# Kernel optimization log

Hardware: AMD Instinct MI355X
Metric: run time of the kernel (lower is better)

Reference implementation:

```python
import jax, jax.numpy as jnp
import numpy as np

N_NODES = 10242  # icosphere level-5 node count
NNZ = 71694      # ~7 nonzeros per row (6 neighbors + self)


def setup_inputs() -> dict:
    key = jax.random.key(0)
    k1, k2, k3, k4, k5 = jax.random.split(key, 5)
    B, T, C, Cout, Ks = 2, 16, 16, 32, 20
    x = jax.random.normal(k1, (B, T, N_NODES, C), dtype=jnp.float32)
    edge_row = jax.random.randint(k2, (NNZ,), 0, N_NODES, dtype=jnp.int32)
    edge_col = jax.random.randint(k3, (NNZ,), 0, N_NODES, dtype=jnp.int32)
    # small values keep the Chebyshev recurrence numerically bounded over Ks steps
    edge_val = jax.random.uniform(k4, (NNZ,), dtype=jnp.float32, minval=-0.2, maxval=0.2)
    W = jax.random.normal(k5, (Cout, C * Ks), dtype=jnp.float32) * 0.02
    return {"x": x, "edge_row": edge_row, "edge_col": edge_col,
            "edge_val": edge_val, "W": W}


def reference(x, edge_row, edge_col, edge_val, W):
    B, T, N, C = x.shape
    Cout, CK = W.shape
    Ks = CK // C

    def spmm(v):  # sparse L @ v, v: [N, F]
        return jax.ops.segment_sum(edge_val[:, None] * v[edge_col], edge_row,
                                   num_segments=N)

    # [B,T,N,C] -> [B*T,N,C] -> [N,C,B*T] -> [N, C*B*T]
    x0 = x.reshape(B * T, N, C).transpose(1, 2, 0).reshape(N, C * B * T)
    x1 = spmm(x0)

    def step(carry, _):
        a, b = carry
        c = 2.0 * spmm(b) - a
        return (b, c), c

    _, rest = jax.lax.scan(step, (x0, x1), None, length=Ks - 2)
    xs = jnp.concatenate([x0[None], x1[None], rest], axis=0)  # [Ks, N, C*B*T]

    xs = xs.reshape(Ks, N, C, B * T).transpose(3, 1, 2, 0)  # [B*T, N, C, Ks]
    xs = xs.reshape(B * T * N, C * Ks)
    out = xs @ W.T  # [B*T*N, Cout]
    return out.reshape(B, T, N, Cout)
```

## Files before the change

### kernel.cpp

```cpp
#include <hip/hip_runtime.h>

#define N_NODES 10242
#define NNZ_E   71694
#define NNZ_PAD_MAX (NNZ_E + 3 * N_NODES)
#define BT      32
#define C_IN    16
#define K_S     20
#define C_OUT   32
#define F       512
typedef unsigned short u16;
typedef unsigned int   u32;

#define RING_ELEMS ((size_t)N_NODES * F)
#define RING_BYTES (RING_ELEMS * 2)
#define R_SLOTS    8

typedef __attribute__((ext_vector_type(8)))  _Float16 half8;
typedef __attribute__((ext_vector_type(16))) float    float16;

__device__ __forceinline__ void unpack8h(uint4 u, float* f) {
    union { uint4 u; _Float16 h[8]; } v; v.u = u;
    #pragma unroll
    for (int i = 0; i < 8; ++i) f[i] = (float)v.h[i];
}
__device__ __forceinline__ uint4 pack8h(const float* f) {
    union { uint4 u; _Float16 h[8]; } v;
    #pragma unroll
    for (int i = 0; i < 8; ++i) v.h[i] = (_Float16)f[i];
    return v.u;
}
__device__ __forceinline__ u16 f2h(float f) {
    union { _Float16 h; u16 u; } v; v.h = (_Float16)f; return v.u;
}


__global__ void zero_kernel(int* p, int n) {
    int i = blockIdx.x * blockDim.x + threadIdx.x;
    if (i < n) p[i] = 0;
}

__global__ void count_kernel(const int* __restrict__ erow, int* cnt) {
    int e = blockIdx.x * blockDim.x + threadIdx.x;
    if (e < NNZ_E) atomicAdd(&cnt[erow[e]], 1);
}

__global__ void scan_kernel(const int* __restrict__ cnt, int* row_ptr, int* cursor) {
    const int T = 256;
    const int chunk = (N_NODES + T - 1) / T;
    __shared__ int part[T];
    int t = threadIdx.x;
    int base = t * chunk;
    int s = 0;
    for (int i = 0; i < chunk; ++i) {
        int idx = base + i;
        if (idx < N_NODES) s += (cnt[idx] + 3) & ~3;
    }
    part[t] = s;
    __syncthreads();
    for (int off = 1; off < T; off <<= 1) {
        int v = (t >= off) ? part[t - off] : 0;
        __syncthreads();
        part[t] += v;
        __syncthreads();
    }
    int run = (t == 0) ? 0 : part[t - 1];
    for (int i = 0; i < chunk; ++i) {
        int idx = base + i;
        if (idx < N_NODES) {
            row_ptr[idx] = run;
            cursor[idx]  = run;
            run += (cnt[idx] + 3) & ~3;
        }
    }
    if (base <= N_NODES && N_NODES < base + chunk) {
        row_ptr[N_NODES] = run;
    }
}

__global__ void scatter_kernel(const int* __restrict__ erow, int* cursor, int* __restrict__ eidx) {
    int e = blockIdx.x * blockDim.x + threadIdx.x;
    if (e < NNZ_E) {
        int p = atomicAdd(&cursor[erow[e]], 1);
        eidx[p] = e;
    }
}

__global__ void sort_rows_kernel(const int* __restrict__ row_ptr, const int* __restrict__ cnt,
                                 int* eidx) {
    int r = blockIdx.x * blockDim.x + threadIdx.x;
    if (r >= N_NODES) return;
    int s = row_ptr[r], e = s + cnt[r];
    for (int i = s + 1; i < e; ++i) {
        int key = eidx[i];
        int j = i - 1;
        while (j >= s && eidx[j] > key) { eidx[j + 1] = eidx[j]; --j; }
        eidx[j + 1] = key;
    }
}

__global__ void fill_csr_kernel(const int* __restrict__ row_ptr, const int* __restrict__ cnt,
                                const int* __restrict__ eidx,
                                const int* __restrict__ ecol, const float* __restrict__ eval,
                                int2* __restrict__ cpack) {
    int r = blockIdx.x * blockDim.x + threadIdx.x;
    if (r >= N_NODES) return;
    int s = row_ptr[r], e = s + cnt[r];
    for (int p = s; p < e; ++p) {
        int ed = eidx[p];
        cpack[p] = make_int2(ecol[ed], __float_as_int(eval[ed]));
    }
}

__global__ void wtfrag_kernel(const float* __restrict__ W, u16* __restrict__ wtfrag) {
    int i = blockIdx.x * blockDim.x + threadIdx.x;
    if (i >= K_S * 64 * 8) return;
    int j    = i & 7;
    int lane = (i >> 3) & 63;
    int k    = i >> 9;
    int cout = lane & 31;
    int c    = ((lane >> 5) << 3) + j;
    wtfrag[i] = f2h(W[cout * (C_IN * K_S) + c * K_S + k]);
}


__global__ __launch_bounds__(256) void transform_kernel(
        const float* __restrict__ x, u16* __restrict__ T0) {
    int g = blockIdx.x * 256 + threadIdx.x;
    int n   = g >> 9;
    int rem = g & 511;
    int bt  = rem >> 4;
    int c   = rem & 15;
    float v = x[((size_t)bt * N_NODES + n) * C_IN + c];
    T0[(size_t)n * F + rem] = f2h(v);
}


__global__ __launch_bounds__(64) void spmm_step_kernel(
        const u16* __restrict__ srcB, const u16* __restrict__ srcA,
        u16* __restrict__ dst,
        const int* __restrict__ row_ptr, const int2* __restrict__ cpack,
        float alpha, float beta) {
    int n = blockIdx.x;
    int lane = threadIdx.x;
    int s = row_ptr[n], e_end = row_ptr[n + 1];

    float a[8] = {0,0,0,0,0,0,0,0};
    if (beta != 0.f) {
        uint4 ua = ((const uint4*)(srcA + (size_t)n * F))[lane];
        unpack8h(ua, a);
    }

    float acc0[8] = {0,0,0,0,0,0,0,0};
    float acc1[8] = {0,0,0,0,0,0,0,0};

    for (int e = s; e < e_end; e += 4) {
        int2 p0 = cpack[e + 0], p1 = cpack[e + 1];
        int2 p2 = cpack[e + 2], p3 = cpack[e + 3];
        uint4 g0 = ((const uint4*)(srcB + (size_t)p0.x * F))[lane];
        uint4 g1 = ((const uint4*)(srcB + (size_t)p1.x * F))[lane];
        uint4 g2 = ((const uint4*)(srcB + (size_t)p2.x * F))[lane];
        uint4 g3 = ((const uint4*)(srcB + (size_t)p3.x * F))[lane];
        float b0[8], b1[8], b2[8], b3[8];
        unpack8h(g0, b0); unpack8h(g1, b1); unpack8h(g2, b2); unpack8h(g3, b3);
        float v0 = __int_as_float(p0.y), v1 = __int_as_float(p1.y);
        float v2 = __int_as_float(p2.y), v3 = __int_as_float(p3.y);
        #pragma unroll
        for (int i = 0; i < 8; ++i) {
            acc0[i] += v0 * b0[i];
            acc1[i] += v1 * b1[i];
            acc0[i] += v2 * b2[i];
            acc1[i] += v3 * b3[i];
        }
    }

    float y[8];
    #pragma unroll
    for (int i = 0; i < 8; ++i)
        y[i] = alpha * (acc0[i] + acc1[i]) + beta * a[i];

    ((uint4*)(dst + (size_t)n * F))[lane] = pack8h(y);
}


__global__ __launch_bounds__(256) void proj_mfma_kernel(
        const u16* __restrict__ ring, int k0, int kcnt,
        const u16* __restrict__ wtfrag, float* __restrict__ out, int accumulate) {
    int wave = threadIdx.x >> 6;
    int lane = threadIdx.x & 63;
    int n = blockIdx.x * 4 + wave;
    if (n >= N_NODES) return;

    int col = lane & 31;
    int grp = lane >> 5;
    size_t aoff = (size_t)n * F + (size_t)col * 16 + grp * 8;

    union { uint4 u; half8 h; } av[8], bv[8];
    #pragma unroll
    for (int j = 0; j < 8; ++j) {
        int jj = (j < kcnt) ? j : 0;
        int k = k0 + jj;
        av[j].u = *(const uint4*)(ring + (size_t)(k % R_SLOTS) * RING_ELEMS + aoff);
        bv[j].u = *(const uint4*)(wtfrag + (size_t)k * 512 + lane * 8);
    }

    float16 acc = {};
    #pragma unroll
    for (int j = 0; j < 8; ++j) {
        if (j < kcnt)
            acc = __builtin_amdgcn_mfma_f32_32x32x16_f16(av[j].h, bv[j].h, acc, 0, 0, 0);
    }

    #pragma unroll
    for (int r = 0; r < 16; ++r) {
        int bt = (r & 3) + 8 * (r >> 2) + 4 * grp;
        float* op = out + ((size_t)bt * N_NODES + n) * C_OUT + col;
        if (accumulate) *op += acc[r];
        else            *op  = acc[r];
    }
}


extern "C" void kernel_launch(void* const* d_in, const int* in_sizes, int n_in,
                              void* d_out, int out_size, void* d_ws, size_t ws_size,
                              hipStream_t stream) {
    const float* x    = (const float*)d_in[0];
    const int*   erow = (const int*)  d_in[1];
    const int*   ecol = (const int*)  d_in[2];
    const float* eval = (const float*)d_in[3];
    const float* W    = (const float*)d_in[4];
    float* out = (float*)d_out;

    char* ws = (char*)d_ws;
    size_t o = 0;
    auto alloc = [&](size_t bytes) -> char* {
        o = (o + 511) & ~(size_t)511;
        char* r = ws + o;
        o += bytes;
        return r;
    };
    int*   cnt     = (int*)  alloc((size_t)N_NODES * 4);
    int*   row_ptr = (int*)  alloc((size_t)(N_NODES + 1) * 4);
    int*   cursor  = (int*)  alloc((size_t)N_NODES * 4);
    int*   eidx    = (int*)  alloc((size_t)NNZ_PAD_MAX * 4);
    int2*  cpack   = (int2*) alloc((size_t)NNZ_PAD_MAX * 8);
    u16*   wtfrag  = (u16*)  alloc((size_t)K_S * 512 * 2);

    u16* ring = (u16*)alloc((size_t)R_SLOTS * RING_BYTES);
    auto slot = [&](int k) -> u16* { return ring + (size_t)(k % R_SLOTS) * RING_ELEMS; };

    zero_kernel<<<(N_NODES + 255) / 256, 256, 0, stream>>>(cnt, N_NODES);
    zero_kernel<<<(2 * NNZ_PAD_MAX + 255) / 256, 256, 0, stream>>>((int*)cpack, 2 * NNZ_PAD_MAX);
    count_kernel<<<(NNZ_E + 255) / 256, 256, 0, stream>>>(erow, cnt);
    scan_kernel<<<1, 256, 0, stream>>>(cnt, row_ptr, cursor);
    scatter_kernel<<<(NNZ_E + 255) / 256, 256, 0, stream>>>(erow, cursor, eidx);
    sort_rows_kernel<<<(N_NODES + 255) / 256, 256, 0, stream>>>(row_ptr, cnt, eidx);
    fill_csr_kernel<<<(N_NODES + 255) / 256, 256, 0, stream>>>(row_ptr, cnt, eidx, ecol, eval, cpack);
    wtfrag_kernel<<<(K_S * 512 + 255) / 256, 256, 0, stream>>>(W, wtfrag);

    const int proj_blocks = (N_NODES + 3) / 4;
    int c0 = 0;
    auto maybe_pass = [&](int k_done) {
        int target = K_S - c0;
        if (target > R_SLOTS) target = R_SLOTS;
        if (target > 0 && (k_done - c0 + 1) == target) {
            proj_mfma_kernel<<<proj_blocks, 256, 0, stream>>>(
                ring, c0, target, wtfrag, out, (c0 > 0) ? 1 : 0);
            c0 += target;
        }
    };

    transform_kernel<<<(int)(RING_ELEMS / 256), 256, 0, stream>>>(x, slot(0));
    maybe_pass(0);

    for (int k = 1; k < K_S; ++k) {
        const u16* srcB = slot(k - 1);
        const u16* srcA = (k >= 2) ? slot(k - 2) : slot(k - 1);
        float alpha = (k == 1) ? 1.f : 2.f;
        float beta  = (k == 1) ? 0.f : -1.f;
        spmm_step_kernel<<<N_NODES, 64, 0, stream>>>(
            srcB, srcA, slot(k), row_ptr, cpack, alpha, beta);
        maybe_pass(k);
    }
}
```

Measured before the change: 491.4 us.

## Fuse CSR build into one block, pad rows to 2, widen ring to 10 slots

Replaces the eight-kernel CSR setup with a single 1024-thread block that counts, scans, scatters, sorts and packs in shared memory, and folds the weight-fragment packing into the transform kernel. Row padding drops from multiples of 4 to multiples of 2, and the SpMM loop is unrolled by 2 to match, cutting wasted zero-edge gathers. The ring grows to 10 slots so the projection runs in two passes instead of three, and the projection kernel now software-pipelines its loads around the MFMA loop. The single-block CSR build serialises setup work on one CU, which may cost more than the launches it removes.

```diff
diff --git a/kernel.cpp b/kernel.cpp
--- a/kernel.cpp
+++ b/kernel.cpp
@@ -2,7 +2,7 @@
 
 #define N_NODES 10242
 #define NNZ_E   71694
-#define NNZ_PAD_MAX (NNZ_E + 3 * N_NODES)
+#define NNZ_PAD_MAX (NNZ_E + N_NODES)
 #define BT      32
 #define C_IN    16
 #define K_S     20
@@ -13,7 +13,7 @@
 
 #define RING_ELEMS ((size_t)N_NODES * F)
 #define RING_BYTES (RING_ELEMS * 2)
-#define R_SLOTS    8
+#define R_SLOTS    10
 
 typedef __attribute__((ext_vector_type(8)))  _Float16 half8;
 typedef __attribute__((ext_vector_type(16))) float    float16;
@@ -34,30 +34,30 @@
 }
 
 
-__global__ void zero_kernel(int* p, int n) {
-    int i = blockIdx.x * blockDim.x + threadIdx.x;
-    if (i < n) p[i] = 0;
-}
-
-__global__ void count_kernel(const int* __restrict__ erow, int* cnt) {
-    int e = blockIdx.x * blockDim.x + threadIdx.x;
-    if (e < NNZ_E) atomicAdd(&cnt[erow[e]], 1);
-}
-
-__global__ void scan_kernel(const int* __restrict__ cnt, int* row_ptr, int* cursor) {
-    const int T = 256;
-    const int chunk = (N_NODES + T - 1) / T;
-    __shared__ int part[T];
+__global__ __launch_bounds__(1024) void csr_build_kernel(
+        const int* __restrict__ erow, const int* __restrict__ ecol,
+        const float* __restrict__ eval,
+        int* __restrict__ row_ptr, int* __restrict__ eidx,
+        int2* __restrict__ cpack) {
+    __shared__ int cur[N_NODES];
+    __shared__ int part[1024];
     int t = threadIdx.x;
+
+    for (int i = t; i < N_NODES; i += 1024) cur[i] = 0;
+    __syncthreads();
+    for (int e = t; e < NNZ_E; e += 1024) atomicAdd(&cur[erow[e]], 1);
+    __syncthreads();
+
+    const int chunk = (N_NODES + 1023) / 1024;
     int base = t * chunk;
     int s = 0;
     for (int i = 0; i < chunk; ++i) {
         int idx = base + i;
-        if (idx < N_NODES) s += (cnt[idx] + 3) & ~3;
+        if (idx < N_NODES) s += (cur[idx] + 1) & ~1;
     }
     part[t] = s;
     __syncthreads();
-    for (int off = 1; off < T; off <<= 1) {
+    for (int off = 1; off < 1024; off <<= 1) {
         int v = (t >= off) ? part[t - off] : 0;
         __syncthreads();
         part[t] += v;
@@ -67,65 +67,52 @@
     for (int i = 0; i < chunk; ++i) {
         int idx = base + i;
         if (idx < N_NODES) {
+            int c = cur[idx];
             row_ptr[idx] = run;
-            cursor[idx]  = run;
-            run += (cnt[idx] + 3) & ~3;
-        }
-    }
-    if (base <= N_NODES && N_NODES < base + chunk) {
-        row_ptr[N_NODES] = run;
-    }
-}
-
-__global__ void scatter_kernel(const int* __restrict__ erow, int* cursor, int* __restrict__ eidx) {
-    int e = blockIdx.x * blockDim.x + threadIdx.x;
-    if (e < NNZ_E) {
-        int p = atomicAdd(&cursor[erow[e]], 1);
+            cur[idx] = run;
+            run += (c + 1) & ~1;
+        }
+    }
+    if (base <= N_NODES && N_NODES < base + chunk) row_ptr[N_NODES] = run;
+    __syncthreads();
+
+    for (int e = t; e < NNZ_E; e += 1024) {
+        int p = atomicAdd(&cur[erow[e]], 1);
         eidx[p] = e;
     }
-}
-
-__global__ void sort_rows_kernel(const int* __restrict__ row_ptr, const int* __restrict__ cnt,
-                                 int* eidx) {
-    int r = blockIdx.x * blockDim.x + threadIdx.x;
-    if (r >= N_NODES) return;
-    int s = row_ptr[r], e = s + cnt[r];
-    for (int i = s + 1; i < e; ++i) {
-        int key = eidx[i];
-        int j = i - 1;
-        while (j >= s && eidx[j] > key) { eidx[j + 1] = eidx[j]; --j; }
-        eidx[j + 1] = key;
-    }
-}
-
-__global__ void fill_csr_kernel(const int* __restrict__ row_ptr, const int* __restrict__ cnt,
-                                const int* __restrict__ eidx,
-                                const int* __restrict__ ecol, const float* __restrict__ eval,
-                                int2* __restrict__ cpack) {
-    int r = blockIdx.x * blockDim.x + threadIdx.x;
-    if (r >= N_NODES) return;
-    int s = row_ptr[r], e = s + cnt[r];
-    for (int p = s; p < e; ++p) {
-        int ed = eidx[p];
-        cpack[p] = make_int2(ecol[ed], __float_as_int(eval[ed]));
-    }
-}
-
-__global__ void wtfrag_kernel(const float* __restrict__ W, u16* __restrict__ wtfrag) {
-    int i = blockIdx.x * blockDim.x + threadIdx.x;
-    if (i >= K_S * 64 * 8) return;
-    int j    = i & 7;
-    int lane = (i >> 3) & 63;
-    int k    = i >> 9;
-    int cout = lane & 31;
-    int c    = ((lane >> 5) << 3) + j;
-    wtfrag[i] = f2h(W[cout * (C_IN * K_S) + c * K_S + k]);
+    __syncthreads();
+
+    for (int r = t; r < N_NODES; r += 1024) {
+        int st = row_ptr[r];
+        int en = cur[r];
+        int pe = row_ptr[r + 1];
+        for (int i = st + 1; i < en; ++i) {
+            int key = eidx[i];
+            int j = i - 1;
+            while (j >= st && eidx[j] > key) { eidx[j + 1] = eidx[j]; --j; }
+            eidx[j + 1] = key;
+        }
+        for (int p = st; p < en; ++p) {
+            int ed = eidx[p];
+            cpack[p] = make_int2(ecol[ed], __float_as_int(eval[ed]));
+        }
+        for (int p = en; p < pe; ++p) cpack[p] = make_int2(0, 0);
+    }
 }
 
 
 __global__ __launch_bounds__(256) void transform_kernel(
-        const float* __restrict__ x, u16* __restrict__ T0) {
+        const float* __restrict__ x, const float* __restrict__ W,
+        u16* __restrict__ T0, u16* __restrict__ wtfrag) {
     int g = blockIdx.x * 256 + threadIdx.x;
+    if (g < K_S * 512) {
+        int j    = g & 7;
+        int lane = (g >> 3) & 63;
+        int k    = g >> 9;
+        int cout = lane & 31;
+        int c    = ((lane >> 5) << 3) + j;
+        wtfrag[g] = f2h(W[cout * (C_IN * K_S) + c * K_S + k]);
+    }
     int n   = g >> 9;
     int rem = g & 511;
     int bt  = rem >> 4;
@@ -144,32 +131,26 @@
     int lane = threadIdx.x;
     int s = row_ptr[n], e_end = row_ptr[n + 1];
 
-    float a[8] = {0,0,0,0,0,0,0,0};
+    float a[8] = {0, 0, 0, 0, 0, 0, 0, 0};
     if (beta != 0.f) {
         uint4 ua = ((const uint4*)(srcA + (size_t)n * F))[lane];
         unpack8h(ua, a);
     }
 
-    float acc0[8] = {0,0,0,0,0,0,0,0};
-    float acc1[8] = {0,0,0,0,0,0,0,0};
-
-    for (int e = s; e < e_end; e += 4) {
-        int2 p0 = cpack[e + 0], p1 = cpack[e + 1];
-        int2 p2 = cpack[e + 2], p3 = cpack[e + 3];
+    float acc0[8] = {0, 0, 0, 0, 0, 0, 0, 0};
+    float acc1[8] = {0, 0, 0, 0, 0, 0, 0, 0};
+
+    for (int e = s; e < e_end; e += 2) {
+        int2 p0 = cpack[e], p1 = cpack[e + 1];
         uint4 g0 = ((const uint4*)(srcB + (size_t)p0.x * F))[lane];
         uint4 g1 = ((const uint4*)(srcB + (size_t)p1.x * F))[lane];
-        uint4 g2 = ((const uint4*)(srcB + (size_t)p2.x * F))[lane];
-        uint4 g3 = ((const uint4*)(srcB + (size_t)p3.x * F))[lane];
-        float b0[8], b1[8], b2[8], b3[8];
-        unpack8h(g0, b0); unpack8h(g1, b1); unpack8h(g2, b2); unpack8h(g3, b3);
+        float b0[8], b1[8];
+        unpack8h(g0, b0); unpack8h(g1, b1);
         float v0 = __int_as_float(p0.y), v1 = __int_as_float(p1.y);
-        float v2 = __int_as_float(p2.y), v3 = __int_as_float(p3.y);
         #pragma unroll
         for (int i = 0; i < 8; ++i) {
             acc0[i] += v0 * b0[i];
             acc1[i] += v1 * b1[i];
-            acc0[i] += v2 * b2[i];
-            acc1[i] += v3 * b3[i];
         }
     }
 
@@ -194,20 +175,21 @@
     int grp = lane >> 5;
     size_t aoff = (size_t)n * F + (size_t)col * 16 + grp * 8;
 
-    union { uint4 u; half8 h; } av[8], bv[8];
-    #pragma unroll
-    for (int j = 0; j < 8; ++j) {
-        int jj = (j < kcnt) ? j : 0;
-        int k = k0 + jj;
-        av[j].u = *(const uint4*)(ring + (size_t)(k % R_SLOTS) * RING_ELEMS + aoff);
-        bv[j].u = *(const uint4*)(wtfrag + (size_t)k * 512 + lane * 8);
-    }
+    union uv { uint4 u; half8 h; };
+    uv av, bv;
+    av.u = *(const uint4*)(ring + (size_t)(k0 % R_SLOTS) * RING_ELEMS + aoff);
+    bv.u = *(const uint4*)(wtfrag + (size_t)k0 * 512 + lane * 8);
 
     float16 acc = {};
-    #pragma unroll
-    for (int j = 0; j < 8; ++j) {
-        if (j < kcnt)
-            acc = __builtin_amdgcn_mfma_f32_32x32x16_f16(av[j].h, bv[j].h, acc, 0, 0, 0);
+    for (int j = 0; j < kcnt; ++j) {
+        uv an = av, bn = bv;
+        if (j + 1 < kcnt) {
+            int k = k0 + j + 1;
+            an.u = *(const uint4*)(ring + (size_t)(k % R_SLOTS) * RING_ELEMS + aoff);
+            bn.u = *(const uint4*)(wtfrag + (size_t)k * 512 + lane * 8);
+        }
+        acc = __builtin_amdgcn_mfma_f32_32x32x16_f16(av.h, bv.h, acc, 0, 0, 0);
+        av = an; bv = bn;
     }
 
     #pragma unroll
@@ -238,24 +220,16 @@
         o += bytes;
         return r;
     };
-    int*   cnt     = (int*)  alloc((size_t)N_NODES * 4);
     int*   row_ptr = (int*)  alloc((size_t)(N_NODES + 1) * 4);
-    int*   cursor  = (int*)  alloc((size_t)N_NODES * 4);
     int*   eidx    = (int*)  alloc((size_t)NNZ_PAD_MAX * 4);
     int2*  cpack   = (int2*) alloc((size_t)NNZ_PAD_MAX * 8);
     u16*   wtfrag  = (u16*)  alloc((size_t)K_S * 512 * 2);
-
-    u16* ring = (u16*)alloc((size_t)R_SLOTS * RING_BYTES);
+    u16*   ring    = (u16*)  alloc((size_t)R_SLOTS * RING_BYTES);
     auto slot = [&](int k) -> u16* { return ring + (size_t)(k % R_SLOTS) * RING_ELEMS; };
 
-    zero_kernel<<<(N_NODES + 255) / 256, 256, 0, stream>>>(cnt, N_NODES);
-    zero_kernel<<<(2 * NNZ_PAD_MAX + 255) / 256, 256, 0, stream>>>((int*)cpack, 2 * NNZ_PAD_MAX);
-    count_kernel<<<(NNZ_E + 255) / 256, 256, 0, stream>>>(erow, cnt);
-    scan_kernel<<<1, 256, 0, stream>>>(cnt, row_ptr, cursor);
-    scatter_kernel<<<(NNZ_E + 255) / 256, 256, 0, stream>>>(erow, cursor, eidx);
-    sort_rows_kernel<<<(N_NODES + 255) / 256, 256, 0, stream>>>(row_ptr, cnt, eidx);
-    fill_csr_kernel<<<(N_NODES + 255) / 256, 256, 0, stream>>>(row_ptr, cnt, eidx, ecol, eval, cpack);
-    wtfrag_kernel<<<(K_S * 512 + 255) / 256, 256, 0, stream>>>(W, wtfrag);
+    csr_build_kernel<<<1, 1024, 0, stream>>>(erow, ecol, eval, row_ptr, eidx, cpack);
+
+    transform_kernel<<<(int)(RING_ELEMS / 256), 256, 0, stream>>>(x, W, slot(0), wtfrag);
 
     const int proj_blocks = (N_NODES + 3) / 4;
     int c0 = 0;
@@ -264,12 +238,11 @@
         if (target > R_SLOTS) target = R_SLOTS;
         if (target > 0 && (k_done - c0 + 1) == target) {
             proj_mfma_kernel<<<proj_blocks, 256, 0, stream>>>(
-                ring, c0, target, wtfrag, out, (c0 > 0) ? 1 : 0);
+                slot(0) ? ring : ring, c0, target, wtfrag, out, (c0 > 0) ? 1 : 0);
             c0 += target;
         }
     };
 
-    transform_kernel<<<(int)(RING_ELEMS / 256), 256, 0, stream>>>(x, slot(0));
     maybe_pass(0);
 
     for (int k = 1; k < K_S; ++k) {
```

New measurement: 674.2 us. 37.2% more time.
